# Kernel tuning notes

Measured on AMD Instinct MI355X. Metric: run time of the kernel, lower is better.

Reference implementation:

```python
import jax, jax.numpy as jnp
import numpy as np
from jax import lax

C = 64
EPS = 1e-5


def _layernorm_c(x, g, b):
    # LayerNorm over channel dim of NCHW tensor (matches nn.LayerNorm([C]) applied on NHWC)
    mu = jnp.mean(x, axis=1, keepdims=True)
    var = jnp.var(x, axis=1, keepdims=True)
    xn = (x - mu) * lax.rsqrt(var + EPS)
    return xn * g[None, :, None, None] + b[None, :, None, None]


def _conv1x1(x, w, b):
    # w: [O, I]
    return jnp.einsum('bihw,oi->bohw', x, w) + b[None, :, None, None]


def _dwconv3x3(x, w, b):
    # depthwise 3x3, w: [C, 3, 3]
    k = w[:, None, :, :]  # OIHW with I=1
    y = lax.conv_general_dilated(x, k, (1, 1), 'SAME',
                                 feature_group_count=w.shape[0],
                                 dimension_numbers=('NCHW', 'OIHW', 'NCHW'))
    return y + b[None, :, None, None]


def setup_inputs() -> dict:
    key = jax.random.key(0)
    ks = jax.random.split(key, 24)
    s = 0.02
    d = {}
    d['x'] = jax.random.normal(ks[0], (4, C, 64, 64), dtype=jnp.float32)
    # CTA params
    d['cta_ln_g'] = jnp.ones((C,), jnp.float32)
    d['cta_ln_b'] = jnp.zeros((C,), jnp.float32)
    d['q_w'] = jax.random.normal(ks[1], (C, C), jnp.float32) * s
    d['q_b'] = jnp.zeros((C,), jnp.float32)
    d['k_w'] = jax.random.normal(ks[2], (C, 3, 3), jnp.float32) * s
    d['k_b'] = jnp.zeros((C,), jnp.float32)
    d['v_w'] = jax.random.normal(ks[3], (C, 3, 3), jnp.float32) * s
    d['v_b'] = jnp.zeros((C,), jnp.float32)
    d['cta_out_w'] = jax.random.normal(ks[4], (C, C), jnp.float32) * s
    d['cta_out_b'] = jnp.zeros((C,), jnp.float32)
    # NLE params
    d['nle_ln_g'] = jnp.ones((C,), jnp.float32)
    d['nle_ln_b'] = jnp.zeros((C,), jnp.float32)
    d['b1_w1'] = jax.random.normal(ks[5], (2 * C, C), jnp.float32) * s
    d['b1_b1'] = jnp.zeros((2 * C,), jnp.float32)
    d['b1_w2'] = jax.random.normal(ks[6], (2 * C, 3, 3), jnp.float32) * s
    d['b1_b2'] = jnp.zeros((2 * C,), jnp.float32)
    d['b2_w1'] = jax.random.normal(ks[7], (2 * C, C), jnp.float32) * s
    d['b2_b1'] = jnp.zeros((2 * C,), jnp.float32)
    d['b2_w2'] = jax.random.normal(ks[8], (2 * C, 3, 3), jnp.float32) * s
    d['b2_b2'] = jnp.zeros((2 * C,), jnp.float32)
    d['nle_out_w'] = jax.random.normal(ks[9], (C, 2 * C), jnp.float32) * s
    d['nle_out_b'] = jnp.zeros((C,), jnp.float32)
    return d


def csam_forward(x, cta_ln_g, cta_ln_b, q_w, q_b, k_w, k_b, v_w, v_b, cta_out_w, cta_out_b,
                 nle_ln_g, nle_ln_b, b1_w1, b1_b1, b1_w2, b1_b2, b2_w1, b2_b1, b2_w2, b2_b2,
                 nle_out_w, nle_out_b):
    B, Cc, H, W = x.shape
    scale = jnp.sqrt(jnp.float32(Cc))
    # --- CTA ---
    xn = _layernorm_c(x, cta_ln_g, cta_ln_b)
    q = _conv1x1(xn, q_w, q_b).reshape(B, Cc, H * W)      # [B,C,N]
    k = _dwconv3x3(xn, k_w, k_b).reshape(B, Cc, H * W)    # [B,C,N]
    v = _dwconv3x3(xn, v_w, v_b).reshape(B, Cc, H * W)    # [B,C,N]
    attn = jnp.einsum('bcn,bcm->bnm', q, k) / scale        # [B,N,N]
    attn = jax.nn.softmax(attn, axis=-1)
    out = jnp.einsum('bnm,bcm->bcn', attn, v).reshape(B, Cc, H, W)
    x_att = _conv1x1(out, cta_out_w, cta_out_b) + x
    # --- NLE ---
    xn2 = _layernorm_c(x_att, nle_ln_g, nle_ln_b)
    br1 = jax.nn.gelu(_dwconv3x3(_conv1x1(xn2, b1_w1, b1_b1), b1_w2, b1_b2), approximate=False)
    br2 = jax.nn.gelu(_dwconv3x3(_conv1x1(xn2, b2_w1, b2_b1), b2_w2, b2_b2), approximate=False)
    nle = _conv1x1(br1 * br2, nle_out_w, nle_out_b)
    return nle + x_att


def reference(x, cta_ln_g, cta_ln_b, q_w, q_b, k_w, k_b, v_w, v_b, cta_out_w, cta_out_b,
              nle_ln_g, nle_ln_b, b1_w1, b1_b1, b1_w2, b1_b2, b2_w1, b2_b1, b2_w2, b2_b2,
              nle_out_w, nle_out_b):
    return csam_forward(x, cta_ln_g, cta_ln_b, q_w, q_b, k_w, k_b, v_w, v_b, cta_out_w, cta_out_b,
                        nle_ln_g, nle_ln_b, b1_w1, b1_b1, b1_w2, b1_b2, b2_w1, b2_b1, b2_w2, b2_b2,
                        nle_out_w, nle_out_b)
```

## Files before the change

kernel.cpp:

```cpp
#include <hip/hip_runtime.h>
#include <hip/hip_bf16.h>
#include <math.h>

#define NPIX 4096
#define CH 64
#define BATCH 4
#define NSPLIT 4

typedef __attribute__((ext_vector_type(8))) short short8;
typedef __attribute__((ext_vector_type(4))) float f32x4;
typedef __attribute__((ext_vector_type(4))) unsigned short us4;
typedef __attribute__((ext_vector_type(4))) unsigned int u32x4;

static __device__ __forceinline__ unsigned short f2bf(float f) {
  union { float f; unsigned u; } v; v.f = f;
  unsigned u = v.u;
  unsigned r = u + 0x7FFF + ((u >> 16) & 1);
  return (unsigned short)(r >> 16);
}
static __device__ __forceinline__ float bf2f(unsigned short u) {
  union { unsigned u; float f; } v; v.u = ((unsigned)u) << 16; return v.f;
}
static __device__ __forceinline__ unsigned cvtpk(float lo, float hi) {
  unsigned r;
  asm("v_cvt_pk_bf16_f32 %0, %1, %2" : "=v"(r) : "v"(lo), "v"(hi));
  return r;
}

__global__ __launch_bounds__(256) void k_ln_q(
    const float* __restrict__ x, const float* __restrict__ lg, const float* __restrict__ lb,
    const float* __restrict__ qw, const float* __restrict__ qb,
    float* __restrict__ xn, unsigned short* __restrict__ Q)
{
  __shared__ float xT[64][64];
  __shared__ unsigned short xB[64][64];
  int tid = threadIdx.x, px = tid & 63, g4 = tid >> 6;
  int idx0 = blockIdx.x * 64;
  int idx = idx0 + px;
  int b = idx >> 12, p = idx & 4095;
  const float* xb = x + (size_t)b * CH * NPIX + p;
  for (int j = 0; j < 16; ++j) { int c = 16 * g4 + j; xT[c][px] = xb[(size_t)c * NPIX]; }
  __syncthreads();
  float xv[64]; float s = 0.f;
#pragma unroll
  for (int c = 0; c < 64; ++c) { xv[c] = xT[c][px]; s += xv[c]; }
  float mu = s * (1.f / 64.f), vs = 0.f;
#pragma unroll
  for (int c = 0; c < 64; ++c) { float d = xv[c] - mu; vs += d * d; }
  float rs = rsqrtf(vs * (1.f / 64.f) + 1e-5f);
#pragma unroll
  for (int c = 0; c < 64; ++c) xv[c] = (xv[c] - mu) * rs * lg[c] + lb[c];

  float* xnb = xn + (size_t)b * CH * NPIX + p;
#define LNQ_WR(C0)                                                             \
  {                                                                            \
    unsigned short t[16];                                                      \
    _Pragma("unroll") for (int j = 0; j < 16; ++j) {                           \
      float v = xv[C0 + j];                                                    \
      xnb[(size_t)(C0 + j) * NPIX] = v;                                        \
      t[j] = f2bf(v);                                                          \
    }                                                                          \
    *(short8*)&xB[px][(((C0 / 8) + 0) ^ (px & 7)) * 8] = *(short8*)t;          \
    *(short8*)&xB[px][(((C0 / 8) + 1) ^ (px & 7)) * 8] = *(short8*)(t + 8);    \
  }
  if (g4 == 0) LNQ_WR(0)
  else if (g4 == 1) LNQ_WR(16)
  else if (g4 == 2) LNQ_WR(32)
  else LNQ_WR(48)
#undef LNQ_WR
  __syncthreads();

  int lane = tid & 63, l15 = lane & 15, gg = lane >> 4;
  short8 af[2];
#pragma unroll
  for (int kc = 0; kc < 2; ++kc) {
    const float* wp = qw + (size_t)(g4 * 16 + l15) * 64 + kc * 32 + 8 * gg;
    unsigned short t[8];
#pragma unroll
    for (int j = 0; j < 8; ++j) t[j] = f2bf(wp[j]);
    af[kc] = *(short8*)t;
  }
  float bv[4];
#pragma unroll
  for (int r = 0; r < 4; ++r) bv[r] = qb[g4 * 16 + 4 * gg + r];
#pragma unroll
  for (int ct = 0; ct < 4; ++ct) {
    f32x4 acc = {bv[0], bv[1], bv[2], bv[3]};
    int row = ct * 16 + l15;
    short8 bf0 = *(const short8*)&xB[row][((0 + gg) ^ (row & 7)) * 8];
    short8 bf1 = *(const short8*)&xB[row][((4 + gg) ^ (row & 7)) * 8];
    acc = __builtin_amdgcn_mfma_f32_16x16x32_bf16(af[0], bf0, acc, 0, 0, 0);
    acc = __builtin_amdgcn_mfma_f32_16x16x32_bf16(af[1], bf1, acc, 0, 0, 0);
    us4 v;
#pragma unroll
    for (int r = 0; r < 4; ++r) v[r] = f2bf(acc[r] * 0.125f);
    *(us4*)(Q + (size_t)(idx0 + row) * 64 + g4 * 16 + 4 * gg) = v;
  }
}

__global__ __launch_bounds__(256) void k_dwkv(
    const float* __restrict__ xn,
    const float* __restrict__ kw, const float* __restrict__ kb,
    const float* __restrict__ vw, const float* __restrict__ vb,
    unsigned short* __restrict__ K, unsigned short* __restrict__ VT)
{
  int idx = blockIdx.x * 256 + threadIdx.x;
  int b = idx >> 12, p = idx & 4095;
  int h = p >> 6, w = p & 63;
  int c0 = blockIdx.y * 8;
  size_t base = (size_t)b * CH * NPIX;
  unsigned short kq[8];
#pragma unroll
  for (int j = 0; j < 8; ++j) {
    int c = c0 + j;
    const float* xc = xn + base + (size_t)c * NPIX;
    float ka = kb[c], va = vb[c];
#pragma unroll
    for (int dy = -1; dy <= 1; ++dy) {
#pragma unroll
      for (int dx = -1; dx <= 1; ++dx) {
        int hh = h + dy, ww = w + dx;
        float xvv = (hh >= 0 && hh < 64 && ww >= 0 && ww < 64) ? xc[hh * 64 + ww] : 0.f;
        int t = (dy + 1) * 3 + (dx + 1);
        ka += kw[c * 9 + t] * xvv;
        va += vw[c * 9 + t] * xvv;
      }
    }
    kq[j] = f2bf(ka);
    VT[((size_t)b * CH + c) * NPIX + p] = f2bf(va);
  }
  *(short8*)(K + (size_t)idx * 64 + c0) = *(short8*)(kq);
}

__global__ __launch_bounds__(256) void k_attn(
    const unsigned short* __restrict__ Q, const unsigned short* __restrict__ K,
    const unsigned short* __restrict__ VT, unsigned short* __restrict__ OPb,
    float* __restrict__ LS)
{
  __shared__ float red[4][16][68];
  __shared__ float lsls[4][4][16];

  int tid = threadIdx.x;
  int wid = tid >> 6, lane = tid & 63;
  int l15 = lane & 15, g = lane >> 4;
  int b = blockIdx.y, split = blockIdx.z;
  int qbase = blockIdx.x * 64;

  const unsigned short* Qb = Q + (size_t)b * NPIX * CH;
  const unsigned short* Kb = K + (size_t)b * NPIX * CH;
  const unsigned short* Vb = VT + (size_t)b * CH * NPIX;

  short8 qf[4][2];
#pragma unroll
  for (int qt = 0; qt < 4; ++qt)
#pragma unroll
    for (int kc = 0; kc < 2; ++kc)
      qf[qt][kc] = *(const short8*)(Qb + (size_t)(qbase + qt * 16 + l15) * CH + kc * 32 + 8 * g);

  f32x4 acc[4][4];
#pragma unroll
  for (int qt = 0; qt < 4; ++qt)
#pragma unroll
    for (int cs = 0; cs < 4; ++cs) acc[qt][cs] = (f32x4){0.f, 0.f, 0.f, 0.f};
  float lsum[4] = {0.f, 0.f, 0.f, 0.f};

  int kperm = 8 * (l15 >> 2) + (l15 & 3);
  int kbase = split * 1024 + wid * 256;

  for (int s = 0; s < 8; ++s) {
    int key0 = kbase + s * 32;
    const unsigned short* kp = Kb + (size_t)(key0 + kperm) * CH + 8 * g;
    short8 kf00 = *(const short8*)(kp);
    short8 kf01 = *(const short8*)(kp + 32);
    short8 kf10 = *(const short8*)(kp + 4 * CH);
    short8 kf11 = *(const short8*)(kp + 4 * CH + 32);
    const unsigned short* vp = Vb + (size_t)l15 * NPIX + key0 + 8 * g;
    short8 vf0 = *(const short8*)(vp);
    short8 vf1 = *(const short8*)(vp + 16 * NPIX);
    short8 vf2 = *(const short8*)(vp + 32 * NPIX);
    short8 vf3 = *(const short8*)(vp + 48 * NPIX);

    __builtin_amdgcn_s_setprio(1);
#pragma unroll
    for (int qt = 0; qt < 4; ++qt) {
      f32x4 s0 = {0.f, 0.f, 0.f, 0.f}, s1 = {0.f, 0.f, 0.f, 0.f};
      s0 = __builtin_amdgcn_mfma_f32_16x16x32_bf16(kf00, qf[qt][0], s0, 0, 0, 0);
      s0 = __builtin_amdgcn_mfma_f32_16x16x32_bf16(kf01, qf[qt][1], s0, 0, 0, 0);
      s1 = __builtin_amdgcn_mfma_f32_16x16x32_bf16(kf10, qf[qt][0], s1, 0, 0, 0);
      s1 = __builtin_amdgcn_mfma_f32_16x16x32_bf16(kf11, qf[qt][1], s1, 0, 0, 0);
      float p0 = __expf(s0[0]), p1 = __expf(s0[1]), p2 = __expf(s0[2]), p3 = __expf(s0[3]);
      float p4 = __expf(s1[0]), p5 = __expf(s1[1]), p6 = __expf(s1[2]), p7 = __expf(s1[3]);
      lsum[qt] += (p0 + p1) + (p2 + p3) + (p4 + p5) + (p6 + p7);
      u32x4 pk;
      pk[0] = cvtpk(p0, p1); pk[1] = cvtpk(p2, p3);
      pk[2] = cvtpk(p4, p5); pk[3] = cvtpk(p6, p7);
      short8 pb = *(short8*)&pk;
      acc[qt][0] = __builtin_amdgcn_mfma_f32_16x16x32_bf16(vf0, pb, acc[qt][0], 0, 0, 0);
      acc[qt][1] = __builtin_amdgcn_mfma_f32_16x16x32_bf16(vf1, pb, acc[qt][1], 0, 0, 0);
      acc[qt][2] = __builtin_amdgcn_mfma_f32_16x16x32_bf16(vf2, pb, acc[qt][2], 0, 0, 0);
      acc[qt][3] = __builtin_amdgcn_mfma_f32_16x16x32_bf16(vf3, pb, acc[qt][3], 0, 0, 0);
    }
    __builtin_amdgcn_s_setprio(0);
  }

#pragma unroll
  for (int qt = 0; qt < 4; ++qt) {
    lsum[qt] += __shfl_xor(lsum[qt], 16, 64);
    lsum[qt] += __shfl_xor(lsum[qt], 32, 64);
  }
  if (g == 0) {
#pragma unroll
    for (int qt = 0; qt < 4; ++qt) lsls[wid][qt][l15] = lsum[qt];
  }

  size_t sb = ((size_t)split * BATCH + b) * NPIX;
#pragma unroll
  for (int qt = 0; qt < 4; ++qt) {
    __syncthreads();
#pragma unroll
    for (int cs = 0; cs < 4; ++cs)
      *(f32x4*)&red[wid][l15][cs * 16 + 4 * g] = acc[qt][cs];
    __syncthreads();
    int q = tid >> 4, ch = (tid & 15) * 4;
    f32x4 v = *(f32x4*)&red[0][q][ch];
    v += *(f32x4*)&red[1][q][ch];
    v += *(f32x4*)&red[2][q][ch];
    v += *(f32x4*)&red[3][q][ch];
    us4 o4;
#pragma unroll
    for (int i = 0; i < 4; ++i) o4[i] = f2bf(v[i]);
    *(us4*)(OPb + (sb + qbase + qt * 16 + q) * 64 + ch) = o4;
  }
  __syncthreads();
  if (tid < 64) {
    int qt = tid >> 4, q = tid & 15;
    LS[sb + qbase + qt * 16 + q] =
        lsls[0][qt][q] + lsls[1][qt][q] + lsls[2][qt][q] + lsls[3][qt][q];
  }
}

__global__ __launch_bounds__(256) void k_reduce(
    const unsigned short* __restrict__ OPb, const float* __restrict__ LSv,
    unsigned short* __restrict__ AOT)
{
  int tid = threadIdx.x;
  size_t e0 = (size_t)blockIdx.x * 4096;
#pragma unroll
  for (int h = 0; h < 2; ++h) {
    int off = (h * 256 + tid) * 8;
    int pix = blockIdx.x * 64 + (off >> 6);
    float sv[8] = {0.f, 0.f, 0.f, 0.f, 0.f, 0.f, 0.f, 0.f};
    float ls = 0.f;
#pragma unroll
    for (int sp = 0; sp < NSPLIT; ++sp) {
      short8 a = *(const short8*)(OPb + (size_t)sp * BATCH * NPIX * 64 + e0 + off);
#pragma unroll
      for (int j = 0; j < 8; ++j) sv[j] += bf2f((unsigned short)a[j]);
      ls += LSv[(size_t)sp * BATCH * NPIX + pix];
    }
    float inv = 1.f / ls;
    unsigned short t[8];
#pragma unroll
    for (int j = 0; j < 8; ++j) t[j] = f2bf(sv[j] * inv);
    *(short8*)(AOT + e0 + off) = *(short8*)t;
  }
}

__global__ __launch_bounds__(256) void k_proj_ln2(
    const unsigned short* __restrict__ AOT, const float* __restrict__ x,
    const float* __restrict__ ow, const float* __restrict__ ob,
    const float* __restrict__ lg, const float* __restrict__ lb,
    float* __restrict__ xatt, unsigned short* __restrict__ xn2T)
{
  __shared__ float sm1[4][4][16], sm2[4][4][16];
  int tid = threadIdx.x;
  int wid = tid >> 6, lane = tid & 63;
  int l15 = lane & 15, g = lane >> 4;
  int b = blockIdx.y, pxb = blockIdx.x * 64;
  const unsigned short* In = AOT + ((size_t)b * NPIX + pxb) * 64;

  short8 af[2];
#pragma unroll
  for (int kc = 0; kc < 2; ++kc) {
    const float* wp = ow + (size_t)(wid * 16 + l15) * 64 + kc * 32 + 8 * g;
    unsigned short t[8];
#pragma unroll
    for (int j = 0; j < 8; ++j) t[j] = f2bf(wp[j]);
    af[kc] = *(short8*)t;
  }
  float bv[4], lgv[4], lbv[4];
#pragma unroll
  for (int r = 0; r < 4; ++r) {
    int o = wid * 16 + 4 * g + r;
    bv[r] = ob[o]; lgv[r] = lg[o]; lbv[r] = lb[o];
  }
  f32x4 acc[4];
#pragma unroll
  for (int ct = 0; ct < 4; ++ct) acc[ct] = (f32x4){bv[0], bv[1], bv[2], bv[3]};
#pragma unroll
  for (int ct = 0; ct < 4; ++ct) {
    short8 bf0 = *(const short8*)(In + (size_t)(ct * 16 + l15) * 64 + 8 * g);
    short8 bf1 = *(const short8*)(In + (size_t)(ct * 16 + l15) * 64 + 32 + 8 * g);
    acc[ct] = __builtin_amdgcn_mfma_f32_16x16x32_bf16(af[0], bf0, acc[ct], 0, 0, 0);
    acc[ct] = __builtin_amdgcn_mfma_f32_16x16x32_bf16(af[1], bf1, acc[ct], 0, 0, 0);
  }

  float xo[4][4];
#pragma unroll
  for (int ct = 0; ct < 4; ++ct) {
    int p = pxb + ct * 16 + l15;
    float s1 = 0.f, s2 = 0.f;
#pragma unroll
    for (int r = 0; r < 4; ++r) {
      int o = wid * 16 + 4 * g + r;
      size_t oi = ((size_t)b * CH + o) * NPIX + p;
      float v = acc[ct][r] + x[oi];
      xatt[oi] = v;
      xo[ct][r] = v;
      s1 += v; s2 += v * v;
    }
    s1 += __shfl_xor(s1, 16, 64); s1 += __shfl_xor(s1, 32, 64);
    s2 += __shfl_xor(s2, 16, 64); s2 += __shfl_xor(s2, 32, 64);
    if (g == 0) { sm1[wid][ct][l15] = s1; sm2[wid][ct][l15] = s2; }
  }
  __syncthreads();
#pragma unroll
  for (int ct = 0; ct < 4; ++ct) {
    int p = pxb + ct * 16 + l15;
    float mu = (sm1[0][ct][l15] + sm1[1][ct][l15] + sm1[2][ct][l15] + sm1[3][ct][l15]) * (1.f / 64.f);
    float ms = (sm2[0][ct][l15] + sm2[1][ct][l15] + sm2[2][ct][l15] + sm2[3][ct][l15]) * (1.f / 64.f);
    float rs = rsqrtf(ms - mu * mu + 1e-5f);
    us4 v4;
#pragma unroll
    for (int r = 0; r < 4; ++r) v4[r] = f2bf((xo[ct][r] - mu) * rs * lgv[r] + lbv[r]);
    *(us4*)(xn2T + ((size_t)b * NPIX + p) * 64 + wid * 16 + 4 * g) = v4;
  }
}

__global__ __launch_bounds__(256) void k_pw_both(
    const unsigned short* __restrict__ xn2T,
    const float* __restrict__ w1, const float* __restrict__ bb1,
    const float* __restrict__ w2, const float* __restrict__ bb2,
    float* __restrict__ t1, float* __restrict__ t2)
{
  int tid = threadIdx.x;
  int wid = tid >> 6, lane = tid & 63;
  int l15 = lane & 15, g = lane >> 4;
  int b = blockIdx.y, pxb = blockIdx.x * 64;
  const unsigned short* In = xn2T + ((size_t)b * NPIX + pxb) * 64;
  const float* W  = (wid & 2) ? w2 : w1;
  const float* bb = (wid & 2) ? bb2 : bb1;
  float* t        = (wid & 2) ? t2 : t1;
  int oh = (wid & 1) * 64;

  short8 af[4][2];
#pragma unroll
  for (int ot = 0; ot < 4; ++ot)
#pragma unroll
    for (int kc = 0; kc < 2; ++kc) {
      const float* wp = W + (size_t)(oh + ot * 16 + l15) * 64 + kc * 32 + 8 * g;
      unsigned short tt[8];
#pragma unroll
      for (int j = 0; j < 8; ++j) tt[j] = f2bf(wp[j]);
      af[ot][kc] = *(short8*)tt;
    }
  f32x4 acc[4][4];
#pragma unroll
  for (int ot = 0; ot < 4; ++ot) {
    float b0 = bb[oh + ot * 16 + 4 * g + 0];
    float b1 = bb[oh + ot * 16 + 4 * g + 1];
    float b2 = bb[oh + ot * 16 + 4 * g + 2];
    float b3 = bb[oh + ot * 16 + 4 * g + 3];
#pragma unroll
    for (int ct = 0; ct < 4; ++ct) acc[ot][ct] = (f32x4){b0, b1, b2, b3};
  }
#pragma unroll
  for (int ct = 0; ct < 4; ++ct) {
    short8 bf0 = *(const short8*)(In + (size_t)(ct * 16 + l15) * 64 + 8 * g);
    short8 bf1 = *(const short8*)(In + (size_t)(ct * 16 + l15) * 64 + 32 + 8 * g);
#pragma unroll
    for (int ot = 0; ot < 4; ++ot) {
      acc[ot][ct] = __builtin_amdgcn_mfma_f32_16x16x32_bf16(af[ot][0], bf0, acc[ot][ct], 0, 0, 0);
      acc[ot][ct] = __builtin_amdgcn_mfma_f32_16x16x32_bf16(af[ot][1], bf1, acc[ot][ct], 0, 0, 0);
    }
  }
#pragma unroll
  for (int ot = 0; ot < 4; ++ot)
#pragma unroll
    for (int ct = 0; ct < 4; ++ct) {
      int p = pxb + ct * 16 + l15;
#pragma unroll
      for (int r = 0; r < 4; ++r) {
        int o = oh + ot * 16 + 4 * g + r;
        t[((size_t)b * 128 + o) * NPIX + p] = acc[ot][ct][r];
      }
    }
}

__global__ __launch_bounds__(256) void k_dwgelu(
    const float* __restrict__ t1, const float* __restrict__ t2,
    const float* __restrict__ w1, const float* __restrict__ bb1,
    const float* __restrict__ w2, const float* __restrict__ bb2,
    unsigned short* __restrict__ g12T)
{
  int idx = blockIdx.x * 256 + threadIdx.x;
  int b = idx >> 12, p = idx & 4095;
  int h = p >> 6, w = p & 63;
  int c0 = blockIdx.y * 8;
  unsigned short outv[8];
#pragma unroll
  for (int j = 0; j < 8; ++j) {
    int c = c0 + j;
    size_t tb = ((size_t)b * 128 + c) * NPIX;
    float a1 = bb1[c], a2 = bb2[c];
#pragma unroll
    for (int dy = -1; dy <= 1; ++dy) {
#pragma unroll
      for (int dx = -1; dx <= 1; ++dx) {
        int hh = h + dy, ww = w + dx;
        bool ok = (hh >= 0 && hh < 64 && ww >= 0 && ww < 64);
        float v1 = ok ? t1[tb + hh * 64 + ww] : 0.f;
        float v2 = ok ? t2[tb + hh * 64 + ww] : 0.f;
        int t = (dy + 1) * 3 + (dx + 1);
        a1 += w1[c * 9 + t] * v1;
        a2 += w2[c * 9 + t] * v2;
      }
    }
    float ge1 = 0.5f * a1 * (1.f + erff(a1 * 0.70710678118654752f));
    float ge2 = 0.5f * a2 * (1.f + erff(a2 * 0.70710678118654752f));
    outv[j] = f2bf(ge1 * ge2);
  }
  *(short8*)(g12T + (size_t)idx * 128 + c0) = *(short8*)outv;
}

__global__ __launch_bounds__(256) void k_out(
    const float* __restrict__ W, const float* __restrict__ bias,
    const unsigned short* __restrict__ InT, const float* __restrict__ res,
    float* __restrict__ outF)
{
  int tid = threadIdx.x;
  int wid = tid >> 6, lane = tid & 63;
  int l15 = lane & 15, g = lane >> 4;
  int b = blockIdx.y, pxb = blockIdx.x * 64;
  const unsigned short* In = InT + ((size_t)b * NPIX + pxb) * 128;

  short8 af[4];
#pragma unroll
  for (int kc = 0; kc < 4; ++kc) {
    const float* wp = W + (size_t)(wid * 16 + l15) * 128 + kc * 32 + 8 * g;
    unsigned short t[8];
#pragma unroll
    for (int j = 0; j < 8; ++j) t[j] = f2bf(wp[j]);
    af[kc] = *(short8*)t;
  }
  float bv[4];
#pragma unroll
  for (int r = 0; r < 4; ++r) bv[r] = bias[wid * 16 + 4 * g + r];
#pragma unroll
  for (int ct = 0; ct < 4; ++ct) {
    f32x4 acc = {bv[0], bv[1], bv[2], bv[3]};
#pragma unroll
    for (int kc = 0; kc < 4; ++kc) {
      short8 bf = *(const short8*)(In + (size_t)(ct * 16 + l15) * 128 + kc * 32 + 8 * g);
      acc = __builtin_amdgcn_mfma_f32_16x16x32_bf16(af[kc], bf, acc, 0, 0, 0);
    }
    int p = pxb + ct * 16 + l15;
#pragma unroll
    for (int r = 0; r < 4; ++r) {
      int o = wid * 16 + 4 * g + r;
      size_t oi = ((size_t)b * CH + o) * NPIX + p;
      outF[oi] = acc[r] + res[oi];
    }
  }
}

extern "C" void kernel_launch(void* const* d_in, const int* in_sizes, int n_in,
                              void* d_out, int out_size, void* d_ws, size_t ws_size,
                              hipStream_t stream) {
  const float* x        = (const float*)d_in[0];
  const float* cta_ln_g = (const float*)d_in[1];
  const float* cta_ln_b = (const float*)d_in[2];
  const float* q_w      = (const float*)d_in[3];
  const float* q_b      = (const float*)d_in[4];
  const float* k_w      = (const float*)d_in[5];
  const float* k_b      = (const float*)d_in[6];
  const float* v_w      = (const float*)d_in[7];
  const float* v_b      = (const float*)d_in[8];
  const float* cta_out_w= (const float*)d_in[9];
  const float* cta_out_b= (const float*)d_in[10];
  const float* nle_ln_g = (const float*)d_in[11];
  const float* nle_ln_b = (const float*)d_in[12];
  const float* b1_w1    = (const float*)d_in[13];
  const float* b1_b1    = (const float*)d_in[14];
  const float* b1_w2    = (const float*)d_in[15];
  const float* b1_b2    = (const float*)d_in[16];
  const float* b2_w1    = (const float*)d_in[17];
  const float* b2_b1    = (const float*)d_in[18];
  const float* b2_w2    = (const float*)d_in[19];
  const float* b2_b2    = (const float*)d_in[20];
  const float* nle_out_w= (const float*)d_in[21];
  const float* nle_out_b= (const float*)d_in[22];

  char* ws = (char*)d_ws;
  float*          xn   = (float*)(ws);
  unsigned short* Qb   = (unsigned short*)(ws + (4u  << 20));
  unsigned short* Kb   = (unsigned short*)(ws + (6u  << 20));
  unsigned short* VTb  = (unsigned short*)(ws + (8u  << 20));
  unsigned short* OPb  = (unsigned short*)(ws + (10u << 20));
  float*          LSb  = (float*)(ws + (18u << 20));
  unsigned short* AOT  = (unsigned short*)(ws + (19u << 20));
  float*          xatt = (float*)(ws + (21u << 20));
  unsigned short* xn2T = (unsigned short*)(ws + (25u << 20));
  float*          t1   = (float*)(ws + (27u << 20));
  float*          t2   = (float*)(ws + (35u << 20));
  unsigned short* g12T = (unsigned short*)(ws);

  k_ln_q     <<<256, 256, 0, stream>>>(x, cta_ln_g, cta_ln_b, q_w, q_b, xn, Qb);
  k_dwkv     <<<dim3(64, 8), 256, 0, stream>>>(xn, k_w, k_b, v_w, v_b, Kb, VTb);
  k_attn     <<<dim3(64, BATCH, NSPLIT), 256, 0, stream>>>(Qb, Kb, VTb, OPb, LSb);
  k_reduce   <<<256, 256, 0, stream>>>(OPb, LSb, AOT);
  k_proj_ln2 <<<dim3(64, 4), 256, 0, stream>>>(AOT, x, cta_out_w, cta_out_b, nle_ln_g, nle_ln_b, xatt, xn2T);
  k_pw_both  <<<dim3(64, 4), 256, 0, stream>>>(xn2T, b1_w1, b1_b1, b2_w1, b2_b1, t1, t2);
  k_dwgelu   <<<dim3(64, 16), 256, 0, stream>>>(t1, t2, b1_w2, b1_b2, b2_w2, b2_b2, g12T);
  k_out      <<<dim3(64, 4), 256, 0, stream>>>(nle_out_w, nle_out_b, g12T, xatt, (float*)d_out);
}
```

Measured before the change: 87.48 us.

## Store intermediates in bf16, double-buffer attention loads, fuse split reduce into projection

The LN output xn and the pointwise intermediates t1/t2 are now stored as bf16 instead of fp32, halving their memory traffic. The attention loop is restructured to prefetch the next K/V fragments into registers while computing the current ones, and the softmax row sum is computed with an extra MFMA against a vector of ones instead of scalar adds plus shuffles. The separate k_reduce kernel is removed; the projection kernel now combines the split partial outputs and normalizes them itself, saving a launch and a round-trip buffer. These changes trade some precision and register pressure for lower bandwidth and overhead.

```diff
diff --git a/kernel.cpp b/kernel.cpp
--- a/kernel.cpp
+++ b/kernel.cpp
@@ -30,7 +30,7 @@
 __global__ __launch_bounds__(256) void k_ln_q(
     const float* __restrict__ x, const float* __restrict__ lg, const float* __restrict__ lb,
     const float* __restrict__ qw, const float* __restrict__ qb,
-    float* __restrict__ xn, unsigned short* __restrict__ Q)
+    unsigned short* __restrict__ xnS, unsigned short* __restrict__ Q)
 {
   __shared__ float xT[64][64];
   __shared__ unsigned short xB[64][64];
@@ -51,14 +51,14 @@
 #pragma unroll
   for (int c = 0; c < 64; ++c) xv[c] = (xv[c] - mu) * rs * lg[c] + lb[c];
 
-  float* xnb = xn + (size_t)b * CH * NPIX + p;
+  unsigned short* xnb = xnS + (size_t)b * CH * NPIX + p;
 #define LNQ_WR(C0)                                                             \
   {                                                                            \
     unsigned short t[16];                                                      \
     _Pragma("unroll") for (int j = 0; j < 16; ++j) {                           \
       float v = xv[C0 + j];                                                    \
-      xnb[(size_t)(C0 + j) * NPIX] = v;                                        \
       t[j] = f2bf(v);                                                          \
+      xnb[(size_t)(C0 + j) * NPIX] = t[j];                                     \
     }                                                                          \
     *(short8*)&xB[px][(((C0 / 8) + 0) ^ (px & 7)) * 8] = *(short8*)t;          \
     *(short8*)&xB[px][(((C0 / 8) + 1) ^ (px & 7)) * 8] = *(short8*)(t + 8);    \
@@ -99,7 +99,7 @@
 }
 
 __global__ __launch_bounds__(256) void k_dwkv(
-    const float* __restrict__ xn,
+    const unsigned short* __restrict__ xnS,
     const float* __restrict__ kw, const float* __restrict__ kb,
     const float* __restrict__ vw, const float* __restrict__ vb,
     unsigned short* __restrict__ K, unsigned short* __restrict__ VT)
@@ -113,14 +113,14 @@
 #pragma unroll
   for (int j = 0; j < 8; ++j) {
     int c = c0 + j;
-    const float* xc = xn + base + (size_t)c * NPIX;
+    const unsigned short* xc = xnS + base + (size_t)c * NPIX;
     float ka = kb[c], va = vb[c];
 #pragma unroll
     for (int dy = -1; dy <= 1; ++dy) {
 #pragma unroll
       for (int dx = -1; dx <= 1; ++dx) {
         int hh = h + dy, ww = w + dx;
-        float xvv = (hh >= 0 && hh < 64 && ww >= 0 && ww < 64) ? xc[hh * 64 + ww] : 0.f;
+        float xvv = (hh >= 0 && hh < 64 && ww >= 0 && ww < 64) ? bf2f(xc[hh * 64 + ww]) : 0.f;
         int t = (dy + 1) * 3 + (dx + 1);
         ka += kw[c * 9 + t] * xvv;
         va += vw[c * 9 + t] * xvv;
@@ -158,59 +158,85 @@
       qf[qt][kc] = *(const short8*)(Qb + (size_t)(qbase + qt * 16 + l15) * CH + kc * 32 + 8 * g);
 
   f32x4 acc[4][4];
-#pragma unroll
-  for (int qt = 0; qt < 4; ++qt)
+  f32x4 lacc[4];
+#pragma unroll
+  for (int qt = 0; qt < 4; ++qt) {
+    lacc[qt] = (f32x4){0.f, 0.f, 0.f, 0.f};
 #pragma unroll
     for (int cs = 0; cs < 4; ++cs) acc[qt][cs] = (f32x4){0.f, 0.f, 0.f, 0.f};
-  float lsum[4] = {0.f, 0.f, 0.f, 0.f};
+  }
+  short8 ones;
+#pragma unroll
+  for (int j = 0; j < 8; ++j) ones[j] = (short)0x3F80;
 
   int kperm = 8 * (l15 >> 2) + (l15 & 3);
   int kbase = split * 1024 + wid * 256;
-
-  for (int s = 0; s < 8; ++s) {
-    int key0 = kbase + s * 32;
-    const unsigned short* kp = Kb + (size_t)(key0 + kperm) * CH + 8 * g;
-    short8 kf00 = *(const short8*)(kp);
-    short8 kf01 = *(const short8*)(kp + 32);
-    short8 kf10 = *(const short8*)(kp + 4 * CH);
-    short8 kf11 = *(const short8*)(kp + 4 * CH + 32);
-    const unsigned short* vp = Vb + (size_t)l15 * NPIX + key0 + 8 * g;
-    short8 vf0 = *(const short8*)(vp);
-    short8 vf1 = *(const short8*)(vp + 16 * NPIX);
-    short8 vf2 = *(const short8*)(vp + 32 * NPIX);
-    short8 vf3 = *(const short8*)(vp + 48 * NPIX);
-
-    __builtin_amdgcn_s_setprio(1);
-#pragma unroll
-    for (int qt = 0; qt < 4; ++qt) {
-      f32x4 s0 = {0.f, 0.f, 0.f, 0.f}, s1 = {0.f, 0.f, 0.f, 0.f};
-      s0 = __builtin_amdgcn_mfma_f32_16x16x32_bf16(kf00, qf[qt][0], s0, 0, 0, 0);
-      s0 = __builtin_amdgcn_mfma_f32_16x16x32_bf16(kf01, qf[qt][1], s0, 0, 0, 0);
-      s1 = __builtin_amdgcn_mfma_f32_16x16x32_bf16(kf10, qf[qt][0], s1, 0, 0, 0);
-      s1 = __builtin_amdgcn_mfma_f32_16x16x32_bf16(kf11, qf[qt][1], s1, 0, 0, 0);
-      float p0 = __expf(s0[0]), p1 = __expf(s0[1]), p2 = __expf(s0[2]), p3 = __expf(s0[3]);
-      float p4 = __expf(s1[0]), p5 = __expf(s1[1]), p6 = __expf(s1[2]), p7 = __expf(s1[3]);
-      lsum[qt] += (p0 + p1) + (p2 + p3) + (p4 + p5) + (p6 + p7);
-      u32x4 pk;
-      pk[0] = cvtpk(p0, p1); pk[1] = cvtpk(p2, p3);
-      pk[2] = cvtpk(p4, p5); pk[3] = cvtpk(p6, p7);
-      short8 pb = *(short8*)&pk;
-      acc[qt][0] = __builtin_amdgcn_mfma_f32_16x16x32_bf16(vf0, pb, acc[qt][0], 0, 0, 0);
-      acc[qt][1] = __builtin_amdgcn_mfma_f32_16x16x32_bf16(vf1, pb, acc[qt][1], 0, 0, 0);
-      acc[qt][2] = __builtin_amdgcn_mfma_f32_16x16x32_bf16(vf2, pb, acc[qt][2], 0, 0, 0);
-      acc[qt][3] = __builtin_amdgcn_mfma_f32_16x16x32_bf16(vf3, pb, acc[qt][3], 0, 0, 0);
-    }
-    __builtin_amdgcn_s_setprio(0);
-  }
-
-#pragma unroll
-  for (int qt = 0; qt < 4; ++qt) {
-    lsum[qt] += __shfl_xor(lsum[qt], 16, 64);
-    lsum[qt] += __shfl_xor(lsum[qt], 32, 64);
-  }
+  const unsigned short* kpl = Kb + (size_t)(kbase + kperm) * CH + 8 * g;
+  const unsigned short* vpl = Vb + (size_t)l15 * NPIX + kbase + 8 * g;
+
+#define LOADK(K0,K1,K2,K3)                                                     \
+  K0 = *(const short8*)(kpl);                                                  \
+  K1 = *(const short8*)(kpl + 32);                                             \
+  K2 = *(const short8*)(kpl + 4 * CH);                                         \
+  K3 = *(const short8*)(kpl + 4 * CH + 32);                                    \
+  kpl += 32 * CH;
+
+#define LOADV(V0,V1,V2,V3)                                                     \
+  V0 = *(const short8*)(vpl);                                                  \
+  V1 = *(const short8*)(vpl + 16 * NPIX);                                      \
+  V2 = *(const short8*)(vpl + 32 * NPIX);                                      \
+  V3 = *(const short8*)(vpl + 48 * NPIX);                                      \
+  vpl += 32;
+
+#define STEP(K00,K01,K10,K11,V0,V1,V2,V3)                                      \
+  __builtin_amdgcn_s_setprio(1);                                               \
+  _Pragma("unroll")                                                            \
+  for (int qt = 0; qt < 4; ++qt) {                                             \
+    f32x4 s0 = {0.f,0.f,0.f,0.f}, s1 = {0.f,0.f,0.f,0.f};                      \
+    s0 = __builtin_amdgcn_mfma_f32_16x16x32_bf16(K00, qf[qt][0], s0, 0, 0, 0); \
+    s0 = __builtin_amdgcn_mfma_f32_16x16x32_bf16(K01, qf[qt][1], s0, 0, 0, 0); \
+    s1 = __builtin_amdgcn_mfma_f32_16x16x32_bf16(K10, qf[qt][0], s1, 0, 0, 0); \
+    s1 = __builtin_amdgcn_mfma_f32_16x16x32_bf16(K11, qf[qt][1], s1, 0, 0, 0); \
+    float p0 = __expf(s0[0]), p1 = __expf(s0[1]);                              \
+    float p2 = __expf(s0[2]), p3 = __expf(s0[3]);                              \
+    float p4 = __expf(s1[0]), p5 = __expf(s1[1]);                              \
+    float p6 = __expf(s1[2]), p7 = __expf(s1[3]);                              \
+    u32x4 pk;                                                                  \
+    pk[0] = cvtpk(p0, p1); pk[1] = cvtpk(p2, p3);                              \
+    pk[2] = cvtpk(p4, p5); pk[3] = cvtpk(p6, p7);                              \
+    short8 pb = *(short8*)&pk;                                                 \
+    acc[qt][0] = __builtin_amdgcn_mfma_f32_16x16x32_bf16(V0, pb, acc[qt][0], 0, 0, 0); \
+    acc[qt][1] = __builtin_amdgcn_mfma_f32_16x16x32_bf16(V1, pb, acc[qt][1], 0, 0, 0); \
+    acc[qt][2] = __builtin_amdgcn_mfma_f32_16x16x32_bf16(V2, pb, acc[qt][2], 0, 0, 0); \
+    acc[qt][3] = __builtin_amdgcn_mfma_f32_16x16x32_bf16(V3, pb, acc[qt][3], 0, 0, 0); \
+    lacc[qt]   = __builtin_amdgcn_mfma_f32_16x16x32_bf16(ones, pb, lacc[qt], 0, 0, 0); \
+  }                                                                            \
+  __builtin_amdgcn_s_setprio(0);
+
+  short8 ka0, ka1, ka2, ka3, va0, va1, va2, va3;
+  short8 kb0, kb1, kb2, kb3, vb0, vb1, vb2, vb3;
+  LOADK(ka0, ka1, ka2, ka3)
+  LOADV(va0, va1, va2, va3)
+#pragma unroll 1
+  for (int s2 = 0; s2 < 3; ++s2) {
+    LOADK(kb0, kb1, kb2, kb3)
+    LOADV(vb0, vb1, vb2, vb3)
+    STEP(ka0, ka1, ka2, ka3, va0, va1, va2, va3)
+    LOADK(ka0, ka1, ka2, ka3)
+    LOADV(va0, va1, va2, va3)
+    STEP(kb0, kb1, kb2, kb3, vb0, vb1, vb2, vb3)
+  }
+  LOADK(kb0, kb1, kb2, kb3)
+  LOADV(vb0, vb1, vb2, vb3)
+  STEP(ka0, ka1, ka2, ka3, va0, va1, va2, va3)
+  STEP(kb0, kb1, kb2, kb3, vb0, vb1, vb2, vb3)
+#undef LOADK
+#undef LOADV
+#undef STEP
+
   if (g == 0) {
 #pragma unroll
-    for (int qt = 0; qt < 4; ++qt) lsls[wid][qt][l15] = lsum[qt];
+    for (int qt = 0; qt < 4; ++qt) lsls[wid][qt][l15] = lacc[qt][0];
   }
 
   size_t sb = ((size_t)split * BATCH + b) * NPIX;
@@ -239,35 +265,9 @@
   }
 }
 
-__global__ __launch_bounds__(256) void k_reduce(
+__global__ __launch_bounds__(256) void k_proj_ln2(
     const unsigned short* __restrict__ OPb, const float* __restrict__ LSv,
-    unsigned short* __restrict__ AOT)
-{
-  int tid = threadIdx.x;
-  size_t e0 = (size_t)blockIdx.x * 4096;
-#pragma unroll
-  for (int h = 0; h < 2; ++h) {
-    int off = (h * 256 + tid) * 8;
-    int pix = blockIdx.x * 64 + (off >> 6);
-    float sv[8] = {0.f, 0.f, 0.f, 0.f, 0.f, 0.f, 0.f, 0.f};
-    float ls = 0.f;
-#pragma unroll
-    for (int sp = 0; sp < NSPLIT; ++sp) {
-      short8 a = *(const short8*)(OPb + (size_t)sp * BATCH * NPIX * 64 + e0 + off);
-#pragma unroll
-      for (int j = 0; j < 8; ++j) sv[j] += bf2f((unsigned short)a[j]);
-      ls += LSv[(size_t)sp * BATCH * NPIX + pix];
-    }
-    float inv = 1.f / ls;
-    unsigned short t[8];
-#pragma unroll
-    for (int j = 0; j < 8; ++j) t[j] = f2bf(sv[j] * inv);
-    *(short8*)(AOT + e0 + off) = *(short8*)t;
-  }
-}
-
-__global__ __launch_bounds__(256) void k_proj_ln2(
-    const unsigned short* __restrict__ AOT, const float* __restrict__ x,
+    const float* __restrict__ x,
     const float* __restrict__ ow, const float* __restrict__ ob,
     const float* __restrict__ lg, const float* __restrict__ lb,
     float* __restrict__ xatt, unsigned short* __restrict__ xn2T)
@@ -277,7 +277,6 @@
   int wid = tid >> 6, lane = tid & 63;
   int l15 = lane & 15, g = lane >> 4;
   int b = blockIdx.y, pxb = blockIdx.x * 64;
-  const unsigned short* In = AOT + ((size_t)b * NPIX + pxb) * 64;
 
   short8 af[2];
 #pragma unroll
@@ -297,10 +296,28 @@
   f32x4 acc[4];
 #pragma unroll
   for (int ct = 0; ct < 4; ++ct) acc[ct] = (f32x4){bv[0], bv[1], bv[2], bv[3]};
+
 #pragma unroll
   for (int ct = 0; ct < 4; ++ct) {
-    short8 bf0 = *(const short8*)(In + (size_t)(ct * 16 + l15) * 64 + 8 * g);
-    short8 bf1 = *(const short8*)(In + (size_t)(ct * 16 + l15) * 64 + 32 + 8 * g);
+    int p = pxb + ct * 16 + l15;
+    float ls = 0.f;
+#pragma unroll
+    for (int sp = 0; sp < NSPLIT; ++sp) ls += LSv[((size_t)sp * BATCH + b) * NPIX + p];
+    float inv = 1.f / ls;
+    float s0[8] = {0,0,0,0,0,0,0,0}, s1[8] = {0,0,0,0,0,0,0,0};
+#pragma unroll
+    for (int sp = 0; sp < NSPLIT; ++sp) {
+      const unsigned short* op = OPb + (((size_t)sp * BATCH + b) * NPIX + p) * 64 + 8 * g;
+      short8 a0 = *(const short8*)(op);
+      short8 a1 = *(const short8*)(op + 32);
+#pragma unroll
+      for (int j = 0; j < 8; ++j) { s0[j] += bf2f((unsigned short)a0[j]); s1[j] += bf2f((unsigned short)a1[j]); }
+    }
+    unsigned short t0[8], t1[8];
+#pragma unroll
+    for (int j = 0; j < 8; ++j) { t0[j] = f2bf(s0[j] * inv); t1[j] = f2bf(s1[j] * inv); }
+    short8 bf0 = *(short8*)t0;
+    short8 bf1 = *(short8*)t1;
     acc[ct] = __builtin_amdgcn_mfma_f32_16x16x32_bf16(af[0], bf0, acc[ct], 0, 0, 0);
     acc[ct] = __builtin_amdgcn_mfma_f32_16x16x32_bf16(af[1], bf1, acc[ct], 0, 0, 0);
   }
@@ -341,7 +358,7 @@
     const unsigned short* __restrict__ xn2T,
     const float* __restrict__ w1, const float* __restrict__ bb1,
     const float* __restrict__ w2, const float* __restrict__ bb2,
-    float* __restrict__ t1, float* __restrict__ t2)
+    unsigned short* __restrict__ t1, unsigned short* __restrict__ t2)
 {
   int tid = threadIdx.x;
   int wid = tid >> 6, lane = tid & 63;
@@ -350,7 +367,7 @@
   const unsigned short* In = xn2T + ((size_t)b * NPIX + pxb) * 64;
   const float* W  = (wid & 2) ? w2 : w1;
   const float* bb = (wid & 2) ? bb2 : bb1;
-  float* t        = (wid & 2) ? t2 : t1;
+  unsigned short* t = (wid & 2) ? t2 : t1;
   int oh = (wid & 1) * 64;
 
   short8 af[4][2];
@@ -392,13 +409,13 @@
 #pragma unroll
       for (int r = 0; r < 4; ++r) {
         int o = oh + ot * 16 + 4 * g + r;
-        t[((size_t)b * 128 + o) * NPIX + p] = acc[ot][ct][r];
+        t[((size_t)b * 128 + o) * NPIX + p] = f2bf(acc[ot][ct][r]);
       }
     }
 }
 
 __global__ __launch_bounds__(256) void k_dwgelu(
-    const float* __restrict__ t1, const float* __restrict__ t2,
+    const unsigned short* __restrict__ t1, const unsigned short* __restrict__ t2,
     const float* __restrict__ w1, const float* __restrict__ bb1,
     const float* __restrict__ w2, const float* __restrict__ bb2,
     unsigned short* __restrict__ g12T)
@@ -419,8 +436,8 @@
       for (int dx = -1; dx <= 1; ++dx) {
         int hh = h + dy, ww = w + dx;
         bool ok = (hh >= 0 && hh < 64 && ww >= 0 && ww < 64);
-        float v1 = ok ? t1[tb + hh * 64 + ww] : 0.f;
-        float v2 = ok ? t2[tb + hh * 64 + ww] : 0.f;
+        float v1 = ok ? bf2f(t1[tb + hh * 64 + ww]) : 0.f;
+        float v2 = ok ? bf2f(t2[tb + hh * 64 + ww]) : 0.f;
         int t = (dy + 1) * 3 + (dx + 1);
         a1 += w1[c * 9 + t] * v1;
         a2 += w2[c * 9 + t] * v2;
@@ -502,24 +519,22 @@
   const float* nle_out_b= (const float*)d_in[22];
 
   char* ws = (char*)d_ws;
-  float*          xn   = (float*)(ws);
-  unsigned short* Qb   = (unsigned short*)(ws + (4u  << 20));
-  unsigned short* Kb   = (unsigned short*)(ws + (6u  << 20));
-  unsigned short* VTb  = (unsigned short*)(ws + (8u  << 20));
-  unsigned short* OPb  = (unsigned short*)(ws + (10u << 20));
-  float*          LSb  = (float*)(ws + (18u << 20));
-  unsigned short* AOT  = (unsigned short*)(ws + (19u << 20));
-  float*          xatt = (float*)(ws + (21u << 20));
-  unsigned short* xn2T = (unsigned short*)(ws + (25u << 20));
-  float*          t1   = (float*)(ws + (27u << 20));
-  float*          t2   = (float*)(ws + (35u << 20));
-  unsigned short* g12T = (unsigned short*)(ws);
-
-  k_ln_q     <<<256, 256, 0, stream>>>(x, cta_ln_g, cta_ln_b, q_w, q_b, xn, Qb);
-  k_dwkv     <<<dim3(64, 8), 256, 0, stream>>>(xn, k_w, k_b, v_w, v_b, Kb, VTb);
+  unsigned short* xnS  = (unsigned short*)(ws);
+  unsigned short* Qb   = (unsigned short*)(ws + (2u  << 20));
+  unsigned short* Kb   = (unsigned short*)(ws + (4u  << 20));
+  unsigned short* VTb  = (unsigned short*)(ws + (6u  << 20));
+  unsigned short* OPb  = (unsigned short*)(ws + (8u  << 20));
+  float*          LSb  = (float*)(ws + (16u << 20));
+  float*          xatt = (float*)(ws + (17u << 20));
+  unsigned short* xn2T = (unsigned short*)(ws + (21u << 20));
+  unsigned short* t1   = (unsigned short*)(ws + (23u << 20));
+  unsigned short* t2   = (unsigned short*)(ws + (27u << 20));
+  unsigned short* g12T = (unsigned short*)(ws + (31u << 20));
+
+  k_ln_q     <<<256, 256, 0, stream>>>(x, cta_ln_g, cta_ln_b, q_w, q_b, xnS, Qb);
+  k_dwkv     <<<dim3(64, 8), 256, 0, stream>>>(xnS, k_w, k_b, v_w, v_b, Kb, VTb);
   k_attn     <<<dim3(64, BATCH, NSPLIT), 256, 0, stream>>>(Qb, Kb, VTb, OPb, LSb);
-  k_reduce   <<<256, 256, 0, stream>>>(OPb, LSb, AOT);
-  k_proj_ln2 <<<dim3(64, 4), 256, 0, stream>>>(AOT, x, cta_out_w, cta_out_b, nle_ln_g, nle_ln_b, xatt, xn2T);
+  k_proj_ln2 <<<dim3(64, 4), 256, 0, stream>>>(OPb, LSb, x, cta_out_w, cta_out_b, nle_ln_g, nle_ln_b, xatt, xn2T);
   k_pw_both  <<<dim3(64, 4), 256, 0, stream>>>(xn2T, b1_w1, b1_b1, b2_w1, b2_b1, t1, t2);
   k_dwgelu   <<<dim3(64, 16), 256, 0, stream>>>(t1, t2, b1_w2, b1_b2, b2_w2, b2_b2, g12T);
   k_out      <<<dim3(64, 4), 256, 0, stream>>>(nle_out_w, nle_out_b, g12T, xatt, (float*)d_out);
```

After: 118.3 us. +35.2%, slower.

## Stage depthwise conv planes in LDS and double-buffer K/V loads in attention

Applied to the files above, without the earlier changes.

Both depthwise 3x3 kernels (K/V and the GELU branch) now load a whole 64x64 channel plane into shared memory and have each thread compute a 16-pixel row strip from register windows. This replaces redundant 9-tap global reads and per-pixel bounds checks. The attention inner loop is restructured with explicit ping-pong register buffers so the next K/V fragments load while the current MFMA step runs. In exchange, writes to the transposed K and g12T outputs become strided 2-byte scatters (stride 64 or 128 elements), and register pressure rises.

```diff
diff --git a/kernel.cpp b/kernel.cpp
--- a/kernel.cpp
+++ b/kernel.cpp
@@ -104,32 +104,56 @@
     const float* __restrict__ vw, const float* __restrict__ vb,
     unsigned short* __restrict__ K, unsigned short* __restrict__ VT)
 {
-  int idx = blockIdx.x * 256 + threadIdx.x;
-  int b = idx >> 12, p = idx & 4095;
-  int h = p >> 6, w = p & 63;
-  int c0 = blockIdx.y * 8;
-  size_t base = (size_t)b * CH * NPIX;
-  unsigned short kq[8];
-#pragma unroll
-  for (int j = 0; j < 8; ++j) {
-    int c = c0 + j;
-    const float* xc = xn + base + (size_t)c * NPIX;
-    float ka = kb[c], va = vb[c];
-#pragma unroll
-    for (int dy = -1; dy <= 1; ++dy) {
-#pragma unroll
-      for (int dx = -1; dx <= 1; ++dx) {
-        int hh = h + dy, ww = w + dx;
-        float xvv = (hh >= 0 && hh < 64 && ww >= 0 && ww < 64) ? xc[hh * 64 + ww] : 0.f;
-        int t = (dy + 1) * 3 + (dx + 1);
-        ka += kw[c * 9 + t] * xvv;
-        va += vw[c * 9 + t] * xvv;
-      }
-    }
-    kq[j] = f2bf(ka);
-    VT[((size_t)b * CH + c) * NPIX + p] = f2bf(va);
-  }
-  *(short8*)(K + (size_t)idx * 64 + c0) = *(short8*)(kq);
+  __shared__ float pl[64][65];
+  int tid = threadIdx.x;
+  int b = blockIdx.x >> 6, c = blockIdx.x & 63;
+  const float* src = xn + ((size_t)b * CH + c) * NPIX;
+#pragma unroll
+  for (int j = 0; j < 16; ++j) {
+    int i = j * 256 + tid;
+    pl[i >> 6][i & 63] = src[i];
+  }
+  __syncthreads();
+  float kwv[9], vwv[9];
+#pragma unroll
+  for (int t = 0; t < 9; ++t) { kwv[t] = kw[c * 9 + t]; vwv[t] = vw[c * 9 + t]; }
+  float kbc = kb[c], vbc = vb[c];
+
+  int h = tid >> 2, w0 = (tid & 3) * 16;
+  int hm = (h > 0) ? h - 1 : 0;
+  int hp = (h < 63) ? h + 1 : 63;
+  bool okm = h > 0, okp = h < 63;
+  float r0[18], r1[18], r2[18];
+#pragma unroll
+  for (int i = 0; i < 18; ++i) {
+    int w = w0 + i - 1;
+    bool okw = (w >= 0) && (w < 64);
+    int wc = okw ? w : 0;
+    r0[i] = (okw && okm) ? pl[hm][wc] : 0.f;
+    r1[i] = okw ? pl[h][wc] : 0.f;
+    r2[i] = (okw && okp) ? pl[hp][wc] : 0.f;
+  }
+  unsigned short kv[16], vv[16];
+#pragma unroll
+  for (int j = 0; j < 16; ++j) {
+    float ka = kbc
+      + kwv[0] * r0[j] + kwv[1] * r0[j + 1] + kwv[2] * r0[j + 2]
+      + kwv[3] * r1[j] + kwv[4] * r1[j + 1] + kwv[5] * r1[j + 2]
+      + kwv[6] * r2[j] + kwv[7] * r2[j + 1] + kwv[8] * r2[j + 2];
+    float va = vbc
+      + vwv[0] * r0[j] + vwv[1] * r0[j + 1] + vwv[2] * r0[j + 2]
+      + vwv[3] * r1[j] + vwv[4] * r1[j + 1] + vwv[5] * r1[j + 2]
+      + vwv[6] * r2[j] + vwv[7] * r2[j + 1] + vwv[8] * r2[j + 2];
+    kv[j] = f2bf(ka);
+    vv[j] = f2bf(va);
+  }
+  int p0 = tid * 16;
+  unsigned short* vdst = VT + ((size_t)b * CH + c) * NPIX + p0;
+  *(short8*)(vdst) = *(short8*)vv;
+  *(short8*)(vdst + 8) = *(short8*)(vv + 8);
+#pragma unroll
+  for (int j = 0; j < 16; ++j)
+    K[(size_t)(b * NPIX + p0 + j) * 64 + c] = kv[j];
 }
 
 __global__ __launch_bounds__(256) void k_attn(
@@ -166,42 +190,68 @@
 
   int kperm = 8 * (l15 >> 2) + (l15 & 3);
   int kbase = split * 1024 + wid * 256;
-
-  for (int s = 0; s < 8; ++s) {
-    int key0 = kbase + s * 32;
-    const unsigned short* kp = Kb + (size_t)(key0 + kperm) * CH + 8 * g;
-    short8 kf00 = *(const short8*)(kp);
-    short8 kf01 = *(const short8*)(kp + 32);
-    short8 kf10 = *(const short8*)(kp + 4 * CH);
-    short8 kf11 = *(const short8*)(kp + 4 * CH + 32);
-    const unsigned short* vp = Vb + (size_t)l15 * NPIX + key0 + 8 * g;
-    short8 vf0 = *(const short8*)(vp);
-    short8 vf1 = *(const short8*)(vp + 16 * NPIX);
-    short8 vf2 = *(const short8*)(vp + 32 * NPIX);
-    short8 vf3 = *(const short8*)(vp + 48 * NPIX);
-
-    __builtin_amdgcn_s_setprio(1);
-#pragma unroll
-    for (int qt = 0; qt < 4; ++qt) {
-      f32x4 s0 = {0.f, 0.f, 0.f, 0.f}, s1 = {0.f, 0.f, 0.f, 0.f};
-      s0 = __builtin_amdgcn_mfma_f32_16x16x32_bf16(kf00, qf[qt][0], s0, 0, 0, 0);
-      s0 = __builtin_amdgcn_mfma_f32_16x16x32_bf16(kf01, qf[qt][1], s0, 0, 0, 0);
-      s1 = __builtin_amdgcn_mfma_f32_16x16x32_bf16(kf10, qf[qt][0], s1, 0, 0, 0);
-      s1 = __builtin_amdgcn_mfma_f32_16x16x32_bf16(kf11, qf[qt][1], s1, 0, 0, 0);
-      float p0 = __expf(s0[0]), p1 = __expf(s0[1]), p2 = __expf(s0[2]), p3 = __expf(s0[3]);
-      float p4 = __expf(s1[0]), p5 = __expf(s1[1]), p6 = __expf(s1[2]), p7 = __expf(s1[3]);
-      lsum[qt] += (p0 + p1) + (p2 + p3) + (p4 + p5) + (p6 + p7);
-      u32x4 pk;
-      pk[0] = cvtpk(p0, p1); pk[1] = cvtpk(p2, p3);
-      pk[2] = cvtpk(p4, p5); pk[3] = cvtpk(p6, p7);
-      short8 pb = *(short8*)&pk;
-      acc[qt][0] = __builtin_amdgcn_mfma_f32_16x16x32_bf16(vf0, pb, acc[qt][0], 0, 0, 0);
-      acc[qt][1] = __builtin_amdgcn_mfma_f32_16x16x32_bf16(vf1, pb, acc[qt][1], 0, 0, 0);
-      acc[qt][2] = __builtin_amdgcn_mfma_f32_16x16x32_bf16(vf2, pb, acc[qt][2], 0, 0, 0);
-      acc[qt][3] = __builtin_amdgcn_mfma_f32_16x16x32_bf16(vf3, pb, acc[qt][3], 0, 0, 0);
-    }
-    __builtin_amdgcn_s_setprio(0);
-  }
+  const unsigned short* kpl = Kb + (size_t)(kbase + kperm) * CH + 8 * g;
+  const unsigned short* vpl = Vb + (size_t)l15 * NPIX + kbase + 8 * g;
+
+#define LOADK(K0,K1,K2,K3)                                                     \
+  K0 = *(const short8*)(kpl);                                                  \
+  K1 = *(const short8*)(kpl + 32);                                             \
+  K2 = *(const short8*)(kpl + 4 * CH);                                         \
+  K3 = *(const short8*)(kpl + 4 * CH + 32);                                    \
+  kpl += 32 * CH;
+
+#define LOADV(V0,V1,V2,V3)                                                     \
+  V0 = *(const short8*)(vpl);                                                  \
+  V1 = *(const short8*)(vpl + 16 * NPIX);                                      \
+  V2 = *(const short8*)(vpl + 32 * NPIX);                                      \
+  V3 = *(const short8*)(vpl + 48 * NPIX);                                      \
+  vpl += 32;
+
+#define STEP(K00,K01,K10,K11,V0,V1,V2,V3)                                      \
+  __builtin_amdgcn_s_setprio(1);                                               \
+  _Pragma("unroll")                                                            \
+  for (int qt = 0; qt < 4; ++qt) {                                             \
+    f32x4 s0 = {0.f,0.f,0.f,0.f}, s1 = {0.f,0.f,0.f,0.f};                      \
+    s0 = __builtin_amdgcn_mfma_f32_16x16x32_bf16(K00, qf[qt][0], s0, 0, 0, 0); \
+    s0 = __builtin_amdgcn_mfma_f32_16x16x32_bf16(K01, qf[qt][1], s0, 0, 0, 0); \
+    s1 = __builtin_amdgcn_mfma_f32_16x16x32_bf16(K10, qf[qt][0], s1, 0, 0, 0); \
+    s1 = __builtin_amdgcn_mfma_f32_16x16x32_bf16(K11, qf[qt][1], s1, 0, 0, 0); \
+    float p0 = __expf(s0[0]), p1 = __expf(s0[1]);                              \
+    float p2 = __expf(s0[2]), p3 = __expf(s0[3]);                              \
+    float p4 = __expf(s1[0]), p5 = __expf(s1[1]);                              \
+    float p6 = __expf(s1[2]), p7 = __expf(s1[3]);                              \
+    lsum[qt] += (p0 + p1) + (p2 + p3) + (p4 + p5) + (p6 + p7);                 \
+    u32x4 pk;                                                                  \
+    pk[0] = cvtpk(p0, p1); pk[1] = cvtpk(p2, p3);                              \
+    pk[2] = cvtpk(p4, p5); pk[3] = cvtpk(p6, p7);                              \
+    short8 pb = *(short8*)&pk;                                                 \
+    acc[qt][0] = __builtin_amdgcn_mfma_f32_16x16x32_bf16(V0, pb, acc[qt][0], 0, 0, 0); \
+    acc[qt][1] = __builtin_amdgcn_mfma_f32_16x16x32_bf16(V1, pb, acc[qt][1], 0, 0, 0); \
+    acc[qt][2] = __builtin_amdgcn_mfma_f32_16x16x32_bf16(V2, pb, acc[qt][2], 0, 0, 0); \
+    acc[qt][3] = __builtin_amdgcn_mfma_f32_16x16x32_bf16(V3, pb, acc[qt][3], 0, 0, 0); \
+  }                                                                            \
+  __builtin_amdgcn_s_setprio(0);
+
+  short8 ka0, ka1, ka2, ka3, kb0, kb1, kb2, kb3;
+  short8 va0, va1, va2, va3, vb0, vb1, vb2, vb3;
+  LOADK(ka0, ka1, ka2, ka3)
+#pragma unroll 1
+  for (int s2 = 0; s2 < 3; ++s2) {
+    LOADV(va0, va1, va2, va3)
+    LOADK(kb0, kb1, kb2, kb3)
+    STEP(ka0, ka1, ka2, ka3, va0, va1, va2, va3)
+    LOADV(vb0, vb1, vb2, vb3)
+    LOADK(ka0, ka1, ka2, ka3)
+    STEP(kb0, kb1, kb2, kb3, vb0, vb1, vb2, vb3)
+  }
+  LOADV(va0, va1, va2, va3)
+  LOADK(kb0, kb1, kb2, kb3)
+  STEP(ka0, ka1, ka2, ka3, va0, va1, va2, va3)
+  LOADV(vb0, vb1, vb2, vb3)
+  STEP(kb0, kb1, kb2, kb3, vb0, vb1, vb2, vb3)
+#undef LOADK
+#undef LOADV
+#undef STEP
 
 #pragma unroll
   for (int qt = 0; qt < 4; ++qt) {
@@ -403,34 +453,72 @@
     const float* __restrict__ w2, const float* __restrict__ bb2,
     unsigned short* __restrict__ g12T)
 {
-  int idx = blockIdx.x * 256 + threadIdx.x;
-  int b = idx >> 12, p = idx & 4095;
-  int h = p >> 6, w = p & 63;
-  int c0 = blockIdx.y * 8;
-  unsigned short outv[8];
-#pragma unroll
-  for (int j = 0; j < 8; ++j) {
-    int c = c0 + j;
-    size_t tb = ((size_t)b * 128 + c) * NPIX;
-    float a1 = bb1[c], a2 = bb2[c];
-#pragma unroll
-    for (int dy = -1; dy <= 1; ++dy) {
-#pragma unroll
-      for (int dx = -1; dx <= 1; ++dx) {
-        int hh = h + dy, ww = w + dx;
-        bool ok = (hh >= 0 && hh < 64 && ww >= 0 && ww < 64);
-        float v1 = ok ? t1[tb + hh * 64 + ww] : 0.f;
-        float v2 = ok ? t2[tb + hh * 64 + ww] : 0.f;
-        int t = (dy + 1) * 3 + (dx + 1);
-        a1 += w1[c * 9 + t] * v1;
-        a2 += w2[c * 9 + t] * v2;
-      }
-    }
-    float ge1 = 0.5f * a1 * (1.f + erff(a1 * 0.70710678118654752f));
-    float ge2 = 0.5f * a2 * (1.f + erff(a2 * 0.70710678118654752f));
-    outv[j] = f2bf(ge1 * ge2);
-  }
-  *(short8*)(g12T + (size_t)idx * 128 + c0) = *(short8*)outv;
+  __shared__ float pl1[64][65], pl2[64][65];
+  int tid = threadIdx.x;
+  int b = blockIdx.x >> 7, c = blockIdx.x & 127;
+  const float* s1p = t1 + ((size_t)b * 128 + c) * NPIX;
+  const float* s2p = t2 + ((size_t)b * 128 + c) * NPIX;
+#pragma unroll
+  for (int j = 0; j < 16; ++j) {
+    int i = j * 256 + tid;
+    pl1[i >> 6][i & 63] = s1p[i];
+    pl2[i >> 6][i & 63] = s2p[i];
+  }
+  __syncthreads();
+  float w1v[9], w2v[9];
+#pragma unroll
+  for (int t = 0; t < 9; ++t) { w1v[t] = w1[c * 9 + t]; w2v[t] = w2[c * 9 + t]; }
+  float b1c = bb1[c], b2c = bb2[c];
+
+  int h = tid >> 2, w0 = (tid & 3) * 16;
+  int hm = (h > 0) ? h - 1 : 0;
+  int hp = (h < 63) ? h + 1 : 63;
+  bool okm = h > 0, okp = h < 63;
+
+  float a1[16], a2[16];
+  {
+    float r0[18], r1[18], r2[18];
+#pragma unroll
+    for (int i = 0; i < 18; ++i) {
+      int w = w0 + i - 1;
+      bool okw = (w >= 0) && (w < 64);
+      int wc = okw ? w : 0;
+      r0[i] = (okw && okm) ? pl1[hm][wc] : 0.f;
+      r1[i] = okw ? pl1[h][wc] : 0.f;
+      r2[i] = (okw && okp) ? pl1[hp][wc] : 0.f;
+    }
+#pragma unroll
+    for (int j = 0; j < 16; ++j)
+      a1[j] = b1c
+        + w1v[0] * r0[j] + w1v[1] * r0[j + 1] + w1v[2] * r0[j + 2]
+        + w1v[3] * r1[j] + w1v[4] * r1[j + 1] + w1v[5] * r1[j + 2]
+        + w1v[6] * r2[j] + w1v[7] * r2[j + 1] + w1v[8] * r2[j + 2];
+  }
+  {
+    float r0[18], r1[18], r2[18];
+#pragma unroll
+    for (int i = 0; i < 18; ++i) {
+      int w = w0 + i - 1;
+      bool okw = (w >= 0) && (w < 64);
+      int wc = okw ? w : 0;
+      r0[i] = (okw && okm) ? pl2[hm][wc] : 0.f;
+      r1[i] = okw ? pl2[h][wc] : 0.f;
+      r2[i] = (okw && okp) ? pl2[hp][wc] : 0.f;
+    }
+#pragma unroll
+    for (int j = 0; j < 16; ++j)
+      a2[j] = b2c
+        + w2v[0] * r0[j] + w2v[1] * r0[j + 1] + w2v[2] * r0[j + 2]
+        + w2v[3] * r1[j] + w2v[4] * r1[j + 1] + w2v[5] * r1[j + 2]
+        + w2v[6] * r2[j] + w2v[7] * r2[j + 1] + w2v[8] * r2[j + 2];
+  }
+  int p0 = tid * 16;
+#pragma unroll
+  for (int j = 0; j < 16; ++j) {
+    float ge1 = 0.5f * a1[j] * (1.f + erff(a1[j] * 0.70710678118654752f));
+    float ge2 = 0.5f * a2[j] * (1.f + erff(a2[j] * 0.70710678118654752f));
+    g12T[(size_t)(b * NPIX + p0 + j) * 128 + c] = f2bf(ge1 * ge2);
+  }
 }
 
 __global__ __launch_bounds__(256) void k_out(
@@ -516,11 +604,11 @@
   unsigned short* g12T = (unsigned short*)(ws);
 
   k_ln_q     <<<256, 256, 0, stream>>>(x, cta_ln_g, cta_ln_b, q_w, q_b, xn, Qb);
-  k_dwkv     <<<dim3(64, 8), 256, 0, stream>>>(xn, k_w, k_b, v_w, v_b, Kb, VTb);
+  k_dwkv     <<<256, 256, 0, stream>>>(xn, k_w, k_b, v_w, v_b, Kb, VTb);
   k_attn     <<<dim3(64, BATCH, NSPLIT), 256, 0, stream>>>(Qb, Kb, VTb, OPb, LSb);
   k_reduce   <<<256, 256, 0, stream>>>(OPb, LSb, AOT);
   k_proj_ln2 <<<dim3(64, 4), 256, 0, stream>>>(AOT, x, cta_out_w, cta_out_b, nle_ln_g, nle_ln_b, xatt, xn2T);
   k_pw_both  <<<dim3(64, 4), 256, 0, stream>>>(xn2T, b1_w1, b1_b1, b2_w1, b2_b1, t1, t2);
-  k_dwgelu   <<<dim3(64, 16), 256, 0, stream>>>(t1, t2, b1_w2, b1_b2, b2_w2, b2_b2, g12T);
+  k_dwgelu   <<<512, 256, 0, stream>>>(t1, t2, b1_w2, b1_b2, b2_w2, b2_b2, g12T);
   k_out      <<<dim3(64, 4), 256, 0, stream>>>(nle_out_w, nle_out_b, g12T, xatt, (float*)d_out);
 }
```

After: 101.5 us. 16.0% more time.
